# Kernel optimization log

Measured on AMD Instinct MI355X. Metric: run time of the kernel, lower is better.

## Reference

```python
import jax, jax.numpy as jnp
import numpy as np

B, T, C, H = 256, 256, 1024, 64

def setup_inputs() -> dict:
    key = jax.random.key(0)
    kx, kk, kq, kv = jax.random.split(key, 4)
    x = jax.random.normal(kx, (B, T, C), dtype=jnp.float32)
    # Dense kernels init'd with normal(stddev=0.02), stored as [in, out] like flax
    Wk = jax.random.normal(kk, (C, H), dtype=jnp.float32) * 0.02
    Wq = jax.random.normal(kq, (C, H), dtype=jnp.float32) * 0.02
    Wv = jax.random.normal(kv, (C, H), dtype=jnp.float32) * 0.02
    return {"x": x, "Wk": Wk, "Wq": Wq, "Wv": Wv}

def reference(x, Wk, Wq, Wv):
    # single-head causal self-attention (eval mode: dropout is identity)
    k = jnp.einsum('btc,ch->bth', x, Wk)      # [B,T,H]
    q = jnp.einsum('btc,ch->bth', x, Wq)      # [B,T,H]
    v = jnp.einsum('btc,ch->bth', x, Wv)      # [B,T,H]
    scale = jnp.asarray(k.shape[-1], k.dtype) ** -0.5
    wei = jnp.einsum('bth,bsh->bts', q, k) * scale  # [B,T,T]
    t = x.shape[1]
    causal = jnp.tril(jnp.ones((t, t), dtype=bool))
    wei = jnp.where(causal, wei, -jnp.inf)
    wei = jax.nn.softmax(wei, axis=-1)
    out = jnp.einsum('bts,bsh->bth', wei, v)  # [B,T,H]
    return out
```

## Files before the change

kernel.cpp:

```cpp
#include <hip/hip_runtime.h>
#include <hip/hip_bf16.h>

typedef float f32x4 __attribute__((ext_vector_type(4)));
typedef short s16x8 __attribute__((ext_vector_type(8)));

__device__ __forceinline__ unsigned short f2bf(float f) {
    union { float f; unsigned u; } v; v.f = f;
    unsigned r = v.u + 0x7FFF + ((v.u >> 16) & 1);
    return (unsigned short)(r >> 16);
}

__global__ void prep_w(const float* __restrict__ Wk, const float* __restrict__ Wq,
                       const float* __restrict__ Wv, unsigned short* __restrict__ wt) {
    int n = blockIdx.x;
    int tid = threadIdx.x;
    const float* src; int col; float sc = 1.0f;
    if (n < 64)       { src = Wq; col = n;       sc = 0.125f; }
    else if (n < 128) { src = Wk; col = n - 64; }
    else              { src = Wv; col = n - 128; }
#pragma unroll
    for (int i = 0; i < 4; i++) {
        int c = i * 256 + tid;
        wt[n * 1024 + c] = f2bf(src[c * 64 + col] * sc);
    }
}

__global__ __launch_bounds__(256) void proj_kernel(const float* __restrict__ x,
                                                   const unsigned short* __restrict__ wt,
                                                   unsigned short* __restrict__ qkv) {
    __shared__ unsigned short xs[128 * 72];

    const int tid  = threadIdx.x;
    const int lane = tid & 63;
    const int wid  = tid >> 6;
    const int quad = lane >> 4;
    const int l15  = lane & 15;
    const int wm   = wid >> 1;
    const int wn   = wid & 1;
    const long blockM = (long)blockIdx.x * 128;

    f32x4 acc[4][6] = {};

    const int srow = tid >> 4;
    const int scol = tid & 15;
    const float* xbase = x + (blockM + srow) * 1024 + scol * 4;

    for (int k0 = 0; k0 < 1024; k0 += 64) {
        __syncthreads();
#pragma unroll
        for (int p = 0; p < 8; p++) {
            const float4 v = *(const float4*)(xbase + (long)p * 16 * 1024 + k0);
            ushort4 bv;
            bv.x = f2bf(v.x); bv.y = f2bf(v.y); bv.z = f2bf(v.z); bv.w = f2bf(v.w);
            *(ushort4*)&xs[(srow + p * 16) * 72 + scol * 4] = bv;
        }
        __syncthreads();
#pragma unroll
        for (int kk = 0; kk < 64; kk += 32) {
            s16x8 a[4], bf[6];
#pragma unroll
            for (int mt = 0; mt < 4; mt++)
                a[mt] = *(const s16x8*)&xs[(wm * 64 + mt * 16 + l15) * 72 + kk + quad * 8];
#pragma unroll
            for (int nt = 0; nt < 6; nt++)
                bf[nt] = *(const s16x8*)&wt[(long)(wn * 96 + nt * 16 + l15) * 1024 + k0 + kk + quad * 8];
#pragma unroll
            for (int mt = 0; mt < 4; mt++)
#pragma unroll
                for (int nt = 0; nt < 6; nt++)
                    acc[mt][nt] = __builtin_amdgcn_mfma_f32_16x16x32_bf16(a[mt], bf[nt], acc[mt][nt], 0, 0, 0);
        }
    }

#pragma unroll
    for (int mt = 0; mt < 4; mt++)
#pragma unroll
        for (int nt = 0; nt < 6; nt++)
#pragma unroll
            for (int r = 0; r < 4; r++) {
                long row = blockM + wm * 64 + mt * 16 + quad * 4 + r;
                int  col = wn * 96 + nt * 16 + l15;
                qkv[row * 192 + col] = f2bf(acc[mt][nt][r]);
            }
}

__global__ __launch_bounds__(256) void attn_kernel(const unsigned short* __restrict__ qkv,
                                                   float* __restrict__ out) {
    __shared__ unsigned short Vt[64 * 264];
    __shared__ unsigned short Pl[4][16 * 56];

    const int tid  = threadIdx.x;
    const int lane = tid & 63;
    const int wid  = tid >> 6;
    const int quad = lane >> 4;
    const int l15  = lane & 15;
    const int b    = blockIdx.x >> 1;
    const int half = blockIdx.x & 1;

    const unsigned short* qb = qkv + (long)b * 256 * 192;

    {
        const int vs = tid >> 2;
        const int vh = (tid & 3) * 16;
        const int npass = half ? 4 : 2;
        for (int p = 0; p < npass; p++) {
            int s = p * 64 + vs;
            const unsigned short* src = qb + s * 192 + 128 + vh;
            s16x8 v0 = *(const s16x8*)src;
            s16x8 v1 = *(const s16x8*)(src + 8);
#pragma unroll
            for (int i = 0; i < 8; i++) Vt[(vh + i) * 264 + s]     = (unsigned short)v0[i];
#pragma unroll
            for (int i = 0; i < 8; i++) Vt[(vh + 8 + i) * 264 + s] = (unsigned short)v1[i];
        }
    }
    __syncthreads();

    const int base = half * 128 + wid * 32;

    s16x8 qf[2][2];
#pragma unroll
    for (int mt = 0; mt < 2; mt++)
#pragma unroll
        for (int ks = 0; ks < 2; ks++)
            qf[mt][ks] = *(const s16x8*)(qb + (long)(base + mt * 16 + l15) * 192 + ks * 32 + quad * 8);

    f32x4 o[2][4] = {};
    float mr[2][4], lr[2][4];
#pragma unroll
    for (int mt = 0; mt < 2; mt++)
#pragma unroll
        for (int r = 0; r < 4; r++) { mr[mt][r] = -1e30f; lr[mt][r] = 0.0f; }

    const int nst = base / 32 + 1;
    for (int st = 0; st < nst; st++) {
        const int s0 = st * 32;
        s16x8 kf[2][2], vf[4];
#pragma unroll
        for (int sub = 0; sub < 2; sub++)
#pragma unroll
            for (int ks = 0; ks < 2; ks++)
                kf[sub][ks] = *(const s16x8*)(qb + (long)(s0 + sub * 16 + l15) * 192 + 64 + ks * 32 + quad * 8);
#pragma unroll
        for (int n = 0; n < 4; n++)
            vf[n] = *(const s16x8*)&Vt[(n * 16 + l15) * 264 + s0 + quad * 8];

#pragma unroll
        for (int mt = 0; mt < 2; mt++) {
            const int tmin = base + mt * 16;
            f32x4 S0 = {0.f, 0.f, 0.f, 0.f}, S1 = {0.f, 0.f, 0.f, 0.f};
            S0 = __builtin_amdgcn_mfma_f32_16x16x32_bf16(qf[mt][0], kf[0][0], S0, 0, 0, 0);
            S0 = __builtin_amdgcn_mfma_f32_16x16x32_bf16(qf[mt][1], kf[0][1], S0, 0, 0, 0);
            S1 = __builtin_amdgcn_mfma_f32_16x16x32_bf16(qf[mt][0], kf[1][0], S1, 0, 0, 0);
            S1 = __builtin_amdgcn_mfma_f32_16x16x32_bf16(qf[mt][1], kf[1][1], S1, 0, 0, 0);

            if (s0 + 31 > tmin) {
#pragma unroll
                for (int r = 0; r < 4; r++) {
                    int t = tmin + quad * 4 + r;
                    if (s0 + l15 > t)      S0[r] = -1e30f;
                    if (s0 + 16 + l15 > t) S1[r] = -1e30f;
                }
            }

            float a4[4];
#pragma unroll
            for (int r = 0; r < 4; r++) {
                float rm = fmaxf(S0[r], S1[r]);
                rm = fmaxf(rm, __shfl_xor(rm, 1));
                rm = fmaxf(rm, __shfl_xor(rm, 2));
                rm = fmaxf(rm, __shfl_xor(rm, 4));
                rm = fmaxf(rm, __shfl_xor(rm, 8));
                float mn = fmaxf(mr[mt][r], rm);
                float al = exp2f((mr[mt][r] - mn) * 1.44269504f);
                mr[mt][r] = mn;
                float p0 = exp2f((S0[r] - mn) * 1.44269504f);
                float p1 = exp2f((S1[r] - mn) * 1.44269504f);
                float rs = p0 + p1;
                rs += __shfl_xor(rs, 1);
                rs += __shfl_xor(rs, 2);
                rs += __shfl_xor(rs, 4);
                rs += __shfl_xor(rs, 8);
                lr[mt][r] = al * lr[mt][r] + rs;
                a4[r] = al;
                Pl[wid][(quad * 4 + r) * 56 + l15]      = f2bf(p0);
                Pl[wid][(quad * 4 + r) * 56 + l15 + 16] = f2bf(p1);
            }
#pragma unroll
            for (int n = 0; n < 4; n++) {
                f32x4 t = o[mt][n];
#pragma unroll
                for (int r = 0; r < 4; r++) t[r] *= a4[r];
                o[mt][n] = t;
            }
            s16x8 pf = *(const s16x8*)&Pl[wid][l15 * 56 + quad * 8];
#pragma unroll
            for (int n = 0; n < 4; n++)
                o[mt][n] = __builtin_amdgcn_mfma_f32_16x16x32_bf16(pf, vf[n], o[mt][n], 0, 0, 0);
        }
    }

#pragma unroll
    for (int mt = 0; mt < 2; mt++) {
        float inv[4];
#pragma unroll
        for (int r = 0; r < 4; r++) inv[r] = 1.0f / lr[mt][r];
#pragma unroll
        for (int n = 0; n < 4; n++)
#pragma unroll
            for (int r = 0; r < 4; r++) {
                long t = (long)b * 256 + base + mt * 16 + quad * 4 + r;
                out[t * 64 + n * 16 + l15] = o[mt][n][r] * inv[r];
            }
    }
}

extern "C" void kernel_launch(void* const* d_in, const int* in_sizes, int n_in,
                              void* d_out, int out_size, void* d_ws, size_t ws_size,
                              hipStream_t stream) {
    const float* x  = (const float*)d_in[0];
    const float* Wk = (const float*)d_in[1];
    const float* Wq = (const float*)d_in[2];
    const float* Wv = (const float*)d_in[3];
    float* out = (float*)d_out;

    unsigned short* wt  = (unsigned short*)d_ws;
    unsigned short* qkv = wt + 192 * 1024;

    prep_w<<<192, 256, 0, stream>>>(Wk, Wq, Wv, wt);
    proj_kernel<<<512, 256, 0, stream>>>(x, wt, qkv);
    attn_kernel<<<512, 256, 0, stream>>>(qkv, out);
}
```

Measured before the change: 427.1 us.

## Fuse QKV projection and causal attention into one kernel per batch

Replaces the separate projection and attention kernels with a single kernel that handles one whole batch per 512-thread block. Each wave projects 32 rows directly from global x, with a register prefetch of the next k-slice in place of LDS staging, and writes Q, K and transposed V into shared memory. Attention then reads them from LDS, with causally balanced row tiles paired as wid and 15-wid. This removes the qkv round trip through global memory and a kernel launch. The cost is only 256 blocks, heavier per-thread register use (24 accumulators plus 12 B fragments), and W being reloaded from global/L2 by every wave.

```diff
diff --git a/kernel.cpp b/kernel.cpp
--- a/kernel.cpp
+++ b/kernel.cpp
@@ -1,8 +1,9 @@
 #include <hip/hip_runtime.h>
-#include <hip/hip_bf16.h>
 
 typedef float f32x4 __attribute__((ext_vector_type(4)));
 typedef short s16x8 __attribute__((ext_vector_type(8)));
+
+#define MFMA16 __builtin_amdgcn_mfma_f32_16x16x32_bf16
 
 __device__ __forceinline__ unsigned short f2bf(float f) {
     union { float f; unsigned u; } v; v.f = f;
@@ -25,139 +26,117 @@
     }
 }
 
-__global__ __launch_bounds__(256) void proj_kernel(const float* __restrict__ x,
-                                                   const unsigned short* __restrict__ wt,
-                                                   unsigned short* __restrict__ qkv) {
-    __shared__ unsigned short xs[128 * 72];
+__global__ __launch_bounds__(512, 2) void fused_kernel(const float* __restrict__ x,
+                                                       const unsigned short* __restrict__ wt,
+                                                       float* __restrict__ out) {
+    __shared__ unsigned short Ql[256 * 72];
+    __shared__ unsigned short Kl[256 * 72];
+    __shared__ unsigned short Vt[64 * 264];
+    __shared__ unsigned short Pl[8][16 * 56];
 
     const int tid  = threadIdx.x;
     const int lane = tid & 63;
     const int wid  = tid >> 6;
     const int quad = lane >> 4;
     const int l15  = lane & 15;
-    const int wm   = wid >> 1;
-    const int wn   = wid & 1;
-    const long blockM = (long)blockIdx.x * 128;
-
-    f32x4 acc[4][6] = {};
-
-    const int srow = tid >> 4;
-    const int scol = tid & 15;
-    const float* xbase = x + (blockM + srow) * 1024 + scol * 4;
-
-    for (int k0 = 0; k0 < 1024; k0 += 64) {
-        __syncthreads();
-#pragma unroll
-        for (int p = 0; p < 8; p++) {
-            const float4 v = *(const float4*)(xbase + (long)p * 16 * 1024 + k0);
-            ushort4 bv;
-            bv.x = f2bf(v.x); bv.y = f2bf(v.y); bv.z = f2bf(v.z); bv.w = f2bf(v.w);
-            *(ushort4*)&xs[(srow + p * 16) * 72 + scol * 4] = bv;
+    const int b    = blockIdx.x;
+    const int m0   = wid * 32;
+
+    const float* xb = x + (long)b * 256 * 1024;
+
+    f32x4 acc[2][12] = {};
+
+    const float* arow0 = xb + (long)(m0 + l15) * 1024 + quad * 8;
+    const float* arow1 = arow0 + 16 * 1024;
+    const unsigned short* wrow = wt + (long)l15 * 1024 + quad * 8;
+
+    float4 pa0 = *(const float4*)(arow0);
+    float4 pa1 = *(const float4*)(arow0 + 4);
+    float4 pa2 = *(const float4*)(arow1);
+    float4 pa3 = *(const float4*)(arow1 + 4);
+
+    for (int k0 = 0; k0 < 1024; k0 += 32) {
+        s16x8 bf[12];
+#pragma unroll
+        for (int nt = 0; nt < 12; nt++)
+            bf[nt] = *(const s16x8*)(wrow + (long)nt * 16 * 1024 + k0);
+
+        s16x8 af0 = { (short)f2bf(pa0.x), (short)f2bf(pa0.y), (short)f2bf(pa0.z), (short)f2bf(pa0.w),
+                      (short)f2bf(pa1.x), (short)f2bf(pa1.y), (short)f2bf(pa1.z), (short)f2bf(pa1.w) };
+        s16x8 af1 = { (short)f2bf(pa2.x), (short)f2bf(pa2.y), (short)f2bf(pa2.z), (short)f2bf(pa2.w),
+                      (short)f2bf(pa3.x), (short)f2bf(pa3.y), (short)f2bf(pa3.z), (short)f2bf(pa3.w) };
+
+        const int kn = (k0 + 32 < 1024) ? k0 + 32 : 0;
+        pa0 = *(const float4*)(arow0 + kn);
+        pa1 = *(const float4*)(arow0 + kn + 4);
+        pa2 = *(const float4*)(arow1 + kn);
+        pa3 = *(const float4*)(arow1 + kn + 4);
+
+#pragma unroll
+        for (int nt = 0; nt < 12; nt++) {
+            acc[0][nt] = MFMA16(af0, bf[nt], acc[0][nt], 0, 0, 0);
+            acc[1][nt] = MFMA16(af1, bf[nt], acc[1][nt], 0, 0, 0);
         }
-        __syncthreads();
-#pragma unroll
-        for (int kk = 0; kk < 64; kk += 32) {
-            s16x8 a[4], bf[6];
-#pragma unroll
-            for (int mt = 0; mt < 4; mt++)
-                a[mt] = *(const s16x8*)&xs[(wm * 64 + mt * 16 + l15) * 72 + kk + quad * 8];
-#pragma unroll
-            for (int nt = 0; nt < 6; nt++)
-                bf[nt] = *(const s16x8*)&wt[(long)(wn * 96 + nt * 16 + l15) * 1024 + k0 + kk + quad * 8];
-#pragma unroll
-            for (int mt = 0; mt < 4; mt++)
-#pragma unroll
-                for (int nt = 0; nt < 6; nt++)
-                    acc[mt][nt] = __builtin_amdgcn_mfma_f32_16x16x32_bf16(a[mt], bf[nt], acc[mt][nt], 0, 0, 0);
+    }
+
+#pragma unroll
+    for (int mt = 0; mt < 2; mt++) {
+#pragma unroll
+        for (int nt = 0; nt < 12; nt++) {
+            if (nt < 4) {
+#pragma unroll
+                for (int r = 0; r < 4; r++)
+                    Ql[(m0 + mt * 16 + quad * 4 + r) * 72 + nt * 16 + l15] = f2bf(acc[mt][nt][r]);
+            } else if (nt < 8) {
+#pragma unroll
+                for (int r = 0; r < 4; r++)
+                    Kl[(m0 + mt * 16 + quad * 4 + r) * 72 + (nt - 4) * 16 + l15] = f2bf(acc[mt][nt][r]);
+            } else {
+                ushort4 pv;
+                pv.x = f2bf(acc[mt][nt][0]); pv.y = f2bf(acc[mt][nt][1]);
+                pv.z = f2bf(acc[mt][nt][2]); pv.w = f2bf(acc[mt][nt][3]);
+                *(ushort4*)&Vt[((nt - 8) * 16 + l15) * 264 + m0 + mt * 16 + quad * 4] = pv;
+            }
         }
     }
-
-#pragma unroll
-    for (int mt = 0; mt < 4; mt++)
-#pragma unroll
-        for (int nt = 0; nt < 6; nt++)
-#pragma unroll
-            for (int r = 0; r < 4; r++) {
-                long row = blockM + wm * 64 + mt * 16 + quad * 4 + r;
-                int  col = wn * 96 + nt * 16 + l15;
-                qkv[row * 192 + col] = f2bf(acc[mt][nt][r]);
-            }
-}
-
-__global__ __launch_bounds__(256) void attn_kernel(const unsigned short* __restrict__ qkv,
-                                                   float* __restrict__ out) {
-    __shared__ unsigned short Vt[64 * 264];
-    __shared__ unsigned short Pl[4][16 * 56];
-
-    const int tid  = threadIdx.x;
-    const int lane = tid & 63;
-    const int wid  = tid >> 6;
-    const int quad = lane >> 4;
-    const int l15  = lane & 15;
-    const int b    = blockIdx.x >> 1;
-    const int half = blockIdx.x & 1;
-
-    const unsigned short* qb = qkv + (long)b * 256 * 192;
-
-    {
-        const int vs = tid >> 2;
-        const int vh = (tid & 3) * 16;
-        const int npass = half ? 4 : 2;
-        for (int p = 0; p < npass; p++) {
-            int s = p * 64 + vs;
-            const unsigned short* src = qb + s * 192 + 128 + vh;
-            s16x8 v0 = *(const s16x8*)src;
-            s16x8 v1 = *(const s16x8*)(src + 8);
-#pragma unroll
-            for (int i = 0; i < 8; i++) Vt[(vh + i) * 264 + s]     = (unsigned short)v0[i];
-#pragma unroll
-            for (int i = 0; i < 8; i++) Vt[(vh + 8 + i) * 264 + s] = (unsigned short)v1[i];
-        }
-    }
     __syncthreads();
 
-    const int base = half * 128 + wid * 32;
-
-    s16x8 qf[2][2];
-#pragma unroll
-    for (int mt = 0; mt < 2; mt++)
-#pragma unroll
-        for (int ks = 0; ks < 2; ks++)
-            qf[mt][ks] = *(const s16x8*)(qb + (long)(base + mt * 16 + l15) * 192 + ks * 32 + quad * 8);
-
-    f32x4 o[2][4] = {};
-    float mr[2][4], lr[2][4];
-#pragma unroll
-    for (int mt = 0; mt < 2; mt++)
-#pragma unroll
-        for (int r = 0; r < 4; r++) { mr[mt][r] = -1e30f; lr[mt][r] = 0.0f; }
-
-    const int nst = base / 32 + 1;
-    for (int st = 0; st < nst; st++) {
-        const int s0 = st * 32;
-        s16x8 kf[2][2], vf[4];
-#pragma unroll
-        for (int sub = 0; sub < 2; sub++)
-#pragma unroll
-            for (int ks = 0; ks < 2; ks++)
-                kf[sub][ks] = *(const s16x8*)(qb + (long)(s0 + sub * 16 + l15) * 192 + 64 + ks * 32 + quad * 8);
-#pragma unroll
-        for (int n = 0; n < 4; n++)
-            vf[n] = *(const s16x8*)&Vt[(n * 16 + l15) * 264 + s0 + quad * 8];
-
-#pragma unroll
-        for (int mt = 0; mt < 2; mt++) {
-            const int tmin = base + mt * 16;
+    unsigned short* Pw = &Pl[wid][0];
+
+#pragma unroll
+    for (int ti = 0; ti < 2; ti++) {
+        const int r0 = (ti == 0 ? wid : 15 - wid) * 16;
+
+        s16x8 qf0 = *(const s16x8*)&Ql[(r0 + l15) * 72 + quad * 8];
+        s16x8 qf1 = *(const s16x8*)&Ql[(r0 + l15) * 72 + 32 + quad * 8];
+
+        f32x4 o[4] = {};
+        float mr[4], lr[4];
+#pragma unroll
+        for (int r = 0; r < 4; r++) { mr[r] = -1e30f; lr[r] = 0.0f; }
+
+        const int nst = (r0 >> 5) + 1;
+        for (int st = 0; st < nst; st++) {
+            const int s0 = st * 32;
+            s16x8 kf00 = *(const s16x8*)&Kl[(s0 + l15) * 72 + quad * 8];
+            s16x8 kf01 = *(const s16x8*)&Kl[(s0 + l15) * 72 + 32 + quad * 8];
+            s16x8 kf10 = *(const s16x8*)&Kl[(s0 + 16 + l15) * 72 + quad * 8];
+            s16x8 kf11 = *(const s16x8*)&Kl[(s0 + 16 + l15) * 72 + 32 + quad * 8];
+            s16x8 vf[4];
+#pragma unroll
+            for (int n = 0; n < 4; n++)
+                vf[n] = *(const s16x8*)&Vt[(n * 16 + l15) * 264 + s0 + quad * 8];
+
             f32x4 S0 = {0.f, 0.f, 0.f, 0.f}, S1 = {0.f, 0.f, 0.f, 0.f};
-            S0 = __builtin_amdgcn_mfma_f32_16x16x32_bf16(qf[mt][0], kf[0][0], S0, 0, 0, 0);
-            S0 = __builtin_amdgcn_mfma_f32_16x16x32_bf16(qf[mt][1], kf[0][1], S0, 0, 0, 0);
-            S1 = __builtin_amdgcn_mfma_f32_16x16x32_bf16(qf[mt][0], kf[1][0], S1, 0, 0, 0);
-            S1 = __builtin_amdgcn_mfma_f32_16x16x32_bf16(qf[mt][1], kf[1][1], S1, 0, 0, 0);
-
-            if (s0 + 31 > tmin) {
+            S0 = MFMA16(qf0, kf00, S0, 0, 0, 0);
+            S0 = MFMA16(qf1, kf01, S0, 0, 0, 0);
+            S1 = MFMA16(qf0, kf10, S1, 0, 0, 0);
+            S1 = MFMA16(qf1, kf11, S1, 0, 0, 0);
+
+            if (s0 + 31 > r0) {
 #pragma unroll
                 for (int r = 0; r < 4; r++) {
-                    int t = tmin + quad * 4 + r;
+                    int t = r0 + quad * 4 + r;
                     if (s0 + l15 > t)      S0[r] = -1e30f;
                     if (s0 + 16 + l15 > t) S1[r] = -1e30f;
                 }
@@ -171,9 +150,9 @@
                 rm = fmaxf(rm, __shfl_xor(rm, 2));
                 rm = fmaxf(rm, __shfl_xor(rm, 4));
                 rm = fmaxf(rm, __shfl_xor(rm, 8));
-                float mn = fmaxf(mr[mt][r], rm);
-                float al = exp2f((mr[mt][r] - mn) * 1.44269504f);
-                mr[mt][r] = mn;
+                float mn = fmaxf(mr[r], rm);
+                float al = exp2f((mr[r] - mn) * 1.44269504f);
+                mr[r] = mn;
                 float p0 = exp2f((S0[r] - mn) * 1.44269504f);
                 float p1 = exp2f((S1[r] - mn) * 1.44269504f);
                 float rs = p0 + p1;
@@ -181,36 +160,33 @@
                 rs += __shfl_xor(rs, 2);
                 rs += __shfl_xor(rs, 4);
                 rs += __shfl_xor(rs, 8);
-                lr[mt][r] = al * lr[mt][r] + rs;
+                lr[r] = al * lr[r] + rs;
                 a4[r] = al;
-                Pl[wid][(quad * 4 + r) * 56 + l15]      = f2bf(p0);
-                Pl[wid][(quad * 4 + r) * 56 + l15 + 16] = f2bf(p1);
+                Pw[(quad * 4 + r) * 56 + l15]      = f2bf(p0);
+                Pw[(quad * 4 + r) * 56 + l15 + 16] = f2bf(p1);
             }
 #pragma unroll
             for (int n = 0; n < 4; n++) {
-                f32x4 t = o[mt][n];
+                f32x4 t = o[n];
 #pragma unroll
                 for (int r = 0; r < 4; r++) t[r] *= a4[r];
-                o[mt][n] = t;
-            }
-            s16x8 pf = *(const s16x8*)&Pl[wid][l15 * 56 + quad * 8];
+                o[n] = t;
+            }
+            s16x8 pf = *(const s16x8*)&Pw[l15 * 56 + quad * 8];
 #pragma unroll
             for (int n = 0; n < 4; n++)
-                o[mt][n] = __builtin_amdgcn_mfma_f32_16x16x32_bf16(pf, vf[n], o[mt][n], 0, 0, 0);
+                o[n] = MFMA16(pf, vf[n], o[n], 0, 0, 0);
         }
-    }
-
-#pragma unroll
-    for (int mt = 0; mt < 2; mt++) {
+
         float inv[4];
 #pragma unroll
-        for (int r = 0; r < 4; r++) inv[r] = 1.0f / lr[mt][r];
+        for (int r = 0; r < 4; r++) inv[r] = 1.0f / lr[r];
 #pragma unroll
         for (int n = 0; n < 4; n++)
 #pragma unroll
             for (int r = 0; r < 4; r++) {
-                long t = (long)b * 256 + base + mt * 16 + quad * 4 + r;
-                out[t * 64 + n * 16 + l15] = o[mt][n][r] * inv[r];
+                long t = (long)b * 256 + r0 + quad * 4 + r;
+                out[t * 64 + n * 16 + l15] = o[n][r] * inv[r];
             }
     }
 }
@@ -224,10 +200,8 @@
     const float* Wv = (const float*)d_in[3];
     float* out = (float*)d_out;
 
-    unsigned short* wt  = (unsigned short*)d_ws;
-    unsigned short* qkv = wt + 192 * 1024;
+    unsigned short* wt = (unsigned short*)d_ws;
 
     prep_w<<<192, 256, 0, stream>>>(Wk, Wq, Wv, wt);
-    proj_kernel<<<512, 256, 0, stream>>>(x, wt, qkv);
-    attn_kernel<<<512, 256, 0, stream>>>(qkv, out);
-}
+    fused_kernel<<<256, 512, 0, stream>>>(x, wt, out);
+}
```

After: 476.5 us. 1.12x slower.
